# Kernel tuning notes

Hardware: AMD Instinct MI355X
Metric: run time of the kernel (lower is better)

## Reference

```python
import jax, jax.numpy as jnp
import numpy as np

D_MODEL = 1024
NUM_HEADS = 16
NUM_KV_HEADS = 4
HEAD_DIM = D_MODEL // NUM_HEADS  # 64
KV_DIM = HEAD_DIM * NUM_KV_HEADS  # 256
B, N = 2, 2048


def setup_inputs() -> dict:
    key = jax.random.key(0)
    ks = jax.random.split(key, 7)
    std = 1.0 / np.sqrt(D_MODEL)
    return {
        "x": jax.random.normal(ks[0], (B, N, D_MODEL), dtype=jnp.float32),
        "cos": jax.random.uniform(ks[1], (N, HEAD_DIM // 2), dtype=jnp.float32),
        "sin": jax.random.uniform(ks[2], (N, HEAD_DIM // 2), dtype=jnp.float32),
        "Wq": jax.random.normal(ks[3], (D_MODEL, D_MODEL), dtype=jnp.float32) * std,
        "Wk": jax.random.normal(ks[4], (D_MODEL, KV_DIM), dtype=jnp.float32) * std,
        "Wv": jax.random.normal(ks[5], (D_MODEL, KV_DIM), dtype=jnp.float32) * std,
        "Wo": jax.random.normal(ks[6], (D_MODEL, D_MODEL), dtype=jnp.float32) * std,
    }


def _rope(t, cos, sin):
    # t: [B, H, N, head_dim]; cos/sin: [N, head_dim//2]
    t1, t2 = t[..., ::2], t[..., 1::2]
    c = cos[None, None]
    s = sin[None, None]
    # NOTE: halves are concatenated (not re-interleaved), faithful to source.
    return jnp.concatenate([t1 * c - t2 * s, t1 * s + t2 * c], axis=-1)


def reference(x, cos, sin, Wq, Wk, Wv, Wo):
    b, n, d = x.shape
    scale = HEAD_DIM ** -0.5
    q = (x @ Wq).reshape(b, n, NUM_HEADS, HEAD_DIM).transpose(0, 2, 1, 3)
    k = (x @ Wk).reshape(b, n, NUM_KV_HEADS, HEAD_DIM).transpose(0, 2, 1, 3)
    v = (x @ Wv).reshape(b, n, NUM_KV_HEADS, HEAD_DIM).transpose(0, 2, 1, 3)
    q = _rope(q, cos, sin)
    k = _rope(k, cos, sin)
    num_rep = NUM_HEADS // NUM_KV_HEADS
    k = jnp.repeat(k, num_rep, axis=1)  # [b, H, n, hd]
    v = jnp.repeat(v, num_rep, axis=1)
    attn = jnp.einsum("bhqd,bhkd->bhqk", q, k) * scale
    attn = jax.nn.softmax(attn, axis=-1)
    out = jnp.einsum("bhqk,bhkd->bhqd", attn, v)
    out = out.transpose(0, 2, 1, 3).reshape(b, n, d)
    return out @ Wo
```

## Files before the change

kernel.cpp:

```cpp
#include <hip/hip_runtime.h>
#include <math.h>

#define D_MODEL 1024
#define NHEADS  16
#define NKV     4
#define HDIM    64
#define KVDIM   256
#define BB      2
#define NN      2048
#define MROWS   (BB*NN)
#define QKVN    1536
#define NTASK   (MROWS*NHEADS)
#define NSPLIT  2

typedef unsigned short ushort_t;
typedef unsigned int uint_t;
typedef float    f32x4 __attribute__((ext_vector_type(4)));
typedef _Float16 h16x8 __attribute__((ext_vector_type(8)));
typedef _Float16 h16x4 __attribute__((ext_vector_type(4)));
typedef __fp16   fp16x2 __attribute__((ext_vector_type(2)));

#define MFMAH(A,B,C)  __builtin_amdgcn_mfma_f32_16x16x32_f16((A),(B),(C),0,0,0)
#define MFMA16(A,B,C) __builtin_amdgcn_mfma_f32_16x16x16f16((A),(B),(C),0,0,0)
#define EXP2(x) __builtin_amdgcn_exp2f(x)

#define GLDS(gp, lp) __builtin_amdgcn_global_load_lds( \
    (const __attribute__((address_space(1))) void*)(gp), \
    (__attribute__((address_space(3))) void*)(lp), 16, 0, 0)

__device__ __forceinline__ ushort_t f2h(float f) {
    _Float16 h = (_Float16)f;
    return *(ushort_t*)&h;
}
__device__ __forceinline__ float h2f(ushort_t u) {
    return (float)(*(const _Float16*)&u);
}
__device__ __forceinline__ uint_t pk2h(float a, float b) {
    fp16x2 v = __builtin_amdgcn_cvt_pkrtz(a, b);
    return *(uint_t*)&v;
}

__global__ __launch_bounds__(256)
void prep_kernel(const float* __restrict__ x, const float* __restrict__ Wq,
                 const float* __restrict__ Wk, const float* __restrict__ Wv,
                 const float* __restrict__ Wo, ushort_t* __restrict__ xb,
                 ushort_t* __restrict__ WqkvT, ushort_t* __restrict__ WoT)
{
    __shared__ float T[32][33];
    int blk = blockIdx.x;
    if (blk < 4096) {
        const int i = blk * 256 + threadIdx.x;
        float4 v = ((const float4*)x)[i];
        uint2 o;
        o.x = pk2h(v.x, v.y);
        o.y = pk2h(v.z, v.w);
        ((uint2*)xb)[i] = o;
        return;
    }
    blk -= 4096;
    const float* src; ushort_t* dst; int N, bx, by;
    if (blk < 1024)      { src = Wq; dst = WqkvT;                            N = D_MODEL; bx = blk & 31; by = blk >> 5; }
    else if (blk < 1280) { blk -= 1024; src = Wk; dst = WqkvT + (size_t)1024 * D_MODEL; N = KVDIM; bx = blk & 7; by = blk >> 3; }
    else if (blk < 1536) { blk -= 1280; src = Wv; dst = WqkvT + (size_t)1280 * D_MODEL; N = KVDIM; bx = blk & 7; by = blk >> 3; }
    else                 { blk -= 1536; src = Wo; dst = WoT;                 N = D_MODEL; bx = blk & 31; by = blk >> 5; }
    const int tx = threadIdx.x & 31, ty = threadIdx.x >> 5;
    const int n0 = bx * 32, k0 = by * 32;
#pragma unroll
    for (int i = 0; i < 4; i++)
        T[ty + i * 8][tx] = src[(size_t)(k0 + ty + i * 8) * N + n0 + tx];
    __syncthreads();
#pragma unroll
    for (int i = 0; i < 4; i++)
        dst[(size_t)(n0 + ty + i * 8) * D_MODEL + k0 + tx] = f2h(T[tx][ty + i * 8]);
}

__global__ __launch_bounds__(256)
void vtrans_kernel(const ushort_t* __restrict__ QKVh, ushort_t* __restrict__ Vt)
{
    __shared__ ushort_t T[32][34];
    const int tx = threadIdx.x & 31, ty = threadIdx.x >> 5;
    const int n0 = blockIdx.x * 32, d0 = blockIdx.y * 32, b = blockIdx.z;
#pragma unroll
    for (int i = 0; i < 4; i++)
        T[ty + i * 8][tx] =
            QKVh[(size_t)(b * NN + n0 + ty + i * 8) * QKVN + 1280 + d0 + tx];
    __syncthreads();
#pragma unroll
    for (int i = 0; i < 4; i++)
        Vt[(size_t)(b * 256 + d0 + ty + i * 8) * NN + n0 + tx] = T[tx][ty + i * 8];
}

#define NQW (MROWS*NHEADS*32)
#define NKW (MROWS*NKV*32)
__global__ __launch_bounds__(256)
void rope_kernel(const ushort_t* __restrict__ QKVh, const float* __restrict__ Cos,
                 const float* __restrict__ Sin, ushort_t* __restrict__ Qb,
                 ushort_t* __restrict__ Kb)
{
    const float SC = 0.125f * 1.44269504f;
    int idx = blockIdx.x * 256 + threadIdx.x;
    if (idx < NQW) {
        const int row = idx >> 9, rem = idx & 511;
        const int h = rem >> 5, j = rem & 31;
        const int b = row >> 11, n = row & (NN - 1);
        const uint_t pr = *(const uint_t*)&QKVh[(size_t)row * QKVN + h * 64 + 2 * j];
        const float e = h2f((ushort_t)pr), o = h2f((ushort_t)(pr >> 16));
        const float c = Cos[n * 32 + j], s = Sin[n * 32 + j];
        ushort_t* dst = Qb + ((size_t)(b * 16 + h) * NN + n) * 64;
        dst[j]      = f2h((e * c - o * s) * SC);
        dst[j + 32] = f2h((e * s + o * c) * SC);
    } else {
        const int i2 = idx - NQW;
        const int row = i2 >> 7, rem = i2 & 127;
        const int h = rem >> 5, j = rem & 31;
        const int b = row >> 11, n = row & (NN - 1);
        const uint_t pr = *(const uint_t*)&QKVh[(size_t)row * QKVN + 1024 + h * 64 + 2 * j];
        const float e = h2f((ushort_t)pr), o = h2f((ushort_t)(pr >> 16));
        const float c = Cos[n * 32 + j], s = Sin[n * 32 + j];
        ushort_t* dst = Kb + ((size_t)(b * 4 + h) * NN + n) * 64;
        dst[j]      = f2h(e * c - o * s);
        dst[j + 32] = f2h(e * s + o * c);
    }
}

__global__ __launch_bounds__(256)
void gemm_qkv(const ushort_t* __restrict__ A, const ushort_t* __restrict__ Bt,
              ushort_t* __restrict__ C, int M, int N, int K)
{
    __shared__ ushort_t As[2][128 * 32];
    __shared__ ushort_t Bs[2][64 * 32];

    const int tid  = threadIdx.x;
    const int wave = tid >> 6, lane = tid & 63;
    const int quad = lane >> 4, l16 = lane & 15;
    const int rowBase = blockIdx.y * 128, colBase = blockIdx.x * 64;
    const int wm = (wave >> 1) * 64, wn = (wave & 1) * 32;

    f32x4 acc[4][2];
    const f32x4 zz = {0.f, 0.f, 0.f, 0.f};
#pragma unroll
    for (int i = 0; i < 4; i++)
#pragma unroll
        for (int j = 0; j < 2; j++) acc[i][j] = zz;

    const int sr = wave * 32 + (lane >> 2);
    const int sc = ((lane & 3) ^ ((lane >> 3) & 3)) * 8;
    const ushort_t* Ag0 = A + (size_t)(rowBase + sr) * K + sc;
    const ushort_t* Ag1 = A + (size_t)(rowBase + sr + 16) * K + sc;
    const int segA0 = (wave * 2 + 0) * 512, segA1 = (wave * 2 + 1) * 512;
    const int br = wave * 16 + (lane >> 2);
    const ushort_t* Bg0 = Bt + (size_t)(colBase + br) * K + sc;
    const int segB = wave * 512;

    const int fcol = (quad ^ ((l16 >> 1) & 3)) * 8;

    GLDS(Ag0, &As[0][segA0]);
    GLDS(Ag1, &As[0][segA1]);
    GLDS(Bg0, &Bs[0][segB]);

    for (int k0 = 0; k0 < K; k0 += 32) {
        const int cur = (k0 >> 5) & 1, nxt = cur ^ 1;
        __syncthreads();
        if (k0 + 32 < K) {
            GLDS(Ag0 + k0 + 32, &As[nxt][segA0]);
            GLDS(Ag1 + k0 + 32, &As[nxt][segA1]);
            GLDS(Bg0 + k0 + 32, &Bs[nxt][segB]);
        }

        h16x8 af[4], bf[2];
#pragma unroll
        for (int mt = 0; mt < 4; mt++)
            af[mt] = *(const h16x8*)&As[cur][(wm + mt * 16 + l16) * 32 + fcol];
#pragma unroll
        for (int nt = 0; nt < 2; nt++)
            bf[nt] = *(const h16x8*)&Bs[cur][(wn + nt * 16 + l16) * 32 + fcol];
#pragma unroll
        for (int mt = 0; mt < 4; mt++)
#pragma unroll
            for (int nt = 0; nt < 2; nt++)
                acc[mt][nt] = MFMAH(af[mt], bf[nt], acc[mt][nt]);
    }

#pragma unroll
    for (int mt = 0; mt < 4; mt++)
#pragma unroll
        for (int nt = 0; nt < 2; nt++) {
            const int row = rowBase + wm + mt * 16 + quad * 4;
            const int col = colBase + wn + nt * 16 + l16;
#pragma unroll
            for (int r = 0; r < 4; r++)
                C[(size_t)(row + r) * N + col] = f2h(acc[mt][nt][r]);
        }
}

__global__ __launch_bounds__(256)
void attn_mfma(const ushort_t* __restrict__ Qb, const ushort_t* __restrict__ Kb,
               const ushort_t* __restrict__ Vt, ushort_t* __restrict__ Pnum,
               float* __restrict__ Pl)
{
    const int qt = blockIdx.x, h = blockIdx.y;
    const int b = blockIdx.z >> 1, chunk = blockIdx.z & 1;
    const int kvh = h >> 2;
    const int tid = threadIdx.x;
    const int wave = tid >> 6, lane = tid & 63;
    const int quad = lane >> 4, l16 = lane & 15;

    __shared__ ushort_t Ks[64][72];
    __shared__ ushort_t Vs[64][72];

    const int row0 = qt * 256 + wave * 64;
    h16x8 qf[4][2];
#pragma unroll
    for (int mt = 0; mt < 4; mt++) {
        const ushort_t* qp =
            Qb + ((size_t)(b * 16 + h) * NN + row0 + mt * 16 + l16) * 64 + quad * 8;
        qf[mt][0] = *(const h16x8*)qp;
        qf[mt][1] = *(const h16x8*)(qp + 32);
    }

    const ushort_t* kbase = Kb + (size_t)(b * 4 + kvh) * NN * 64;
    const ushort_t* vbase = Vt + (size_t)(b * 256 + kvh * 64) * NN;
    const int key_lo = chunk * (NN / NSPLIT);
    const int rot = (qt + ((h & 3) << 2)) & 15;

    const int srow = tid >> 2, sseg = (tid & 3) * 8;

    const f32x4 zz = {0.f, 0.f, 0.f, 0.f};
    f32x4 o[4][4];
#pragma unroll
    for (int mt = 0; mt < 4; mt++)
#pragma unroll
        for (int dt = 0; dt < 4; dt++) o[mt][dt] = zz;
    float lacc[4] = {0.f, 0.f, 0.f, 0.f};

    int key0 = key_lo + rot * 64;
    const ushort_t* kp0 = kbase + (size_t)(key0 + srow) * 64 + sseg;
    const ushort_t* vp0 = vbase + (size_t)srow * NN + key0 + sseg;
    uint4 kreg0 = *(const uint4*)kp0;
    uint4 kreg1 = *(const uint4*)(kp0 + 32);
    uint4 vreg0 = *(const uint4*)vp0;
    uint4 vreg1 = *(const uint4*)(vp0 + 32);

    for (int t = 0; t < 16; t++) {
        __syncthreads();
        *(uint4*)&Ks[srow][sseg]      = kreg0;
        *(uint4*)&Ks[srow][sseg + 32] = kreg1;
        *(uint4*)&Vs[srow][sseg]      = vreg0;
        *(uint4*)&Vs[srow][sseg + 32] = vreg1;
        __syncthreads();

        if (t < 15) {
            const int kn = key_lo + ((rot + t + 1) & 15) * 64;
            const ushort_t* kpn = kbase + (size_t)(kn + srow) * 64 + sseg;
            const ushort_t* vpn = vbase + (size_t)srow * NN + kn + sseg;
            kreg0 = *(const uint4*)kpn;
            kreg1 = *(const uint4*)(kpn + 32);
            vreg0 = *(const uint4*)vpn;
            vreg1 = *(const uint4*)(vpn + 32);
        }

#pragma unroll
        for (int kt = 0; kt < 4; kt++) {
            h16x8 kf0 = *(const h16x8*)&Ks[kt * 16 + l16][quad * 8];
            h16x8 kf1 = *(const h16x8*)&Ks[kt * 16 + l16][32 + quad * 8];
            h16x4 va[4];
#pragma unroll
            for (int dt = 0; dt < 4; dt++)
                va[dt] = *(const h16x4*)&Vs[dt * 16 + l16][kt * 16 + quad * 4];

            uint2 pb[4];
#pragma unroll
            for (int mt = 0; mt < 4; mt++) {
                f32x4 st = MFMAH(kf0, qf[mt][0], zz);
                st = MFMAH(kf1, qf[mt][1], st);
                const float p0 = EXP2(st[0]);
                const float p1 = EXP2(st[1]);
                const float p2 = EXP2(st[2]);
                const float p3 = EXP2(st[3]);
                lacc[mt] += (p0 + p1) + (p2 + p3);
                pb[mt].x = pk2h(p0, p1);
                pb[mt].y = pk2h(p2, p3);
            }
#pragma unroll
            for (int mt = 0; mt < 4; mt++) {
                const h16x4 pbv = *(const h16x4*)&pb[mt];
#pragma unroll
                for (int dt = 0; dt < 4; dt++)
                    o[mt][dt] = MFMA16(va[dt], pbv, o[mt][dt]);
            }
        }
    }

#pragma unroll
    for (int mt = 0; mt < 4; mt++) {
        lacc[mt] += __shfl_xor(lacc[mt], 16, 64);
        lacc[mt] += __shfl_xor(lacc[mt], 32, 64);
    }

    const size_t task0 = (size_t)(b * 16 + h) * NN + row0;
    ushort_t* np = Pnum + ((size_t)chunk * NTASK + task0) * 64;
#pragma unroll
    for (int mt = 0; mt < 4; mt++) {
        const float inv = 1.0f / lacc[mt];
#pragma unroll
        for (int dt = 0; dt < 4; dt++) {
            f32x4 v = o[mt][dt];
            uint2 pk;
            pk.x = pk2h(v[0] * inv, v[1] * inv);
            pk.y = pk2h(v[2] * inv, v[3] * inv);
            *(uint2*)&np[(size_t)(mt * 16 + l16) * 64 + dt * 16 + quad * 4] = pk;
        }
        if (quad == 0)
            Pl[(size_t)chunk * NTASK + task0 + mt * 16 + l16] = lacc[mt];
    }
}

__global__ __launch_bounds__(256)
void gemm_wo(const ushort_t* __restrict__ Pnum, const float* __restrict__ Pl,
             const ushort_t* __restrict__ WoT, float* __restrict__ C)
{
    __shared__ ushort_t As[2][128 * 40];
    __shared__ ushort_t Bs[2][64 * 32];

    const int tid  = threadIdx.x;
    const int wave = tid >> 6, lane = tid & 63;
    const int quad = lane >> 4, l16 = lane & 15;
    const int rowBase = blockIdx.y * 128, colBase = blockIdx.x * 64;
    const int wm = (wave >> 1) * 64, wn = (wave & 1) * 32;

    f32x4 acc[4][2];
    const f32x4 zz = {0.f, 0.f, 0.f, 0.f};
#pragma unroll
    for (int i = 0; i < 4; i++)
#pragma unroll
        for (int j = 0; j < 2; j++) acc[i][j] = zz;

    const int r0 = tid >> 2;
    const int c8 = (tid & 3) * 8;
    const int bB = rowBase >> 11;
    const int n0 = (rowBase & (NN - 1)) + r0;

    const int br = wave * 16 + (lane >> 2);
    const int sc = ((lane & 3) ^ ((lane >> 3) & 3)) * 8;
    const ushort_t* Bg0 = WoT + (size_t)(colBase + br) * D_MODEL + sc;
    const int segB = wave * 512;
    const int fcol = (quad ^ ((l16 >> 1) & 3)) * 8;

    uint4 a0c0, a0c1, a1c0, a1c1;
    float l00, l01, l10, l11;
#define PREFA(k0) { \
        const int h_ = (k0) >> 6; \
        const int d_ = ((k0) & 63) + c8; \
        const size_t t0_ = ((size_t)(bB * 16 + h_) << 11) + n0; \
        const size_t t1_ = t0_ + 64; \
        a0c0 = *(const uint4*)&Pnum[t0_ * 64 + d_]; \
        a0c1 = *(const uint4*)&Pnum[((size_t)NTASK + t0_) * 64 + d_]; \
        a1c0 = *(const uint4*)&Pnum[t1_ * 64 + d_]; \
        a1c1 = *(const uint4*)&Pnum[((size_t)NTASK + t1_) * 64 + d_]; \
        l00 = Pl[t0_]; l01 = Pl[NTASK + t0_]; \
        l10 = Pl[t1_]; l11 = Pl[NTASK + t1_]; \
    }

    PREFA(0);
    GLDS(Bg0, &Bs[0][segB]);

    for (int k0 = 0; k0 < D_MODEL; k0 += 32) {
        const int cur = (k0 >> 5) & 1, nxt = cur ^ 1;
        __syncthreads();

        {
            const float i0 = 1.f / (l00 + l01), w00 = l00 * i0, w01 = l01 * i0;
            const float i1 = 1.f / (l10 + l11), w10 = l10 * i1, w11 = l11 * i1;
            uint4 o0, o1;
            const uint_t* p0 = (const uint_t*)&a0c0;
            const uint_t* p1 = (const uint_t*)&a0c1;
            const uint_t* q0 = (const uint_t*)&a1c0;
            const uint_t* q1 = (const uint_t*)&a1c1;
            uint_t* po = (uint_t*)&o0;
            uint_t* qo = (uint_t*)&o1;
#pragma unroll
            for (int j = 0; j < 4; j++) {
                fp16x2 u = *(const fp16x2*)&p0[j];
                fp16x2 v = *(const fp16x2*)&p1[j];
                po[j] = pk2h(w00 * (float)u.x + w01 * (float)v.x,
                             w00 * (float)u.y + w01 * (float)v.y);
                fp16x2 s = *(const fp16x2*)&q0[j];
                fp16x2 r = *(const fp16x2*)&q1[j];
                qo[j] = pk2h(w10 * (float)s.x + w11 * (float)r.x,
                             w10 * (float)s.y + w11 * (float)r.y);
            }
            *(uint4*)&As[cur][r0 * 40 + c8]        = o0;
            *(uint4*)&As[cur][(r0 + 64) * 40 + c8] = o1;
        }
        __syncthreads();

        if (k0 + 32 < D_MODEL) {
            GLDS(Bg0 + k0 + 32, &Bs[nxt][segB]);
            PREFA(k0 + 32);
        }

        h16x8 af[4], bf[2];
#pragma unroll
        for (int mt = 0; mt < 4; mt++)
            af[mt] = *(const h16x8*)&As[cur][(wm + mt * 16 + l16) * 40 + quad * 8];
#pragma unroll
        for (int nt = 0; nt < 2; nt++)
            bf[nt] = *(const h16x8*)&Bs[cur][(wn + nt * 16 + l16) * 32 + fcol];
#pragma unroll
        for (int mt = 0; mt < 4; mt++)
#pragma unroll
            for (int nt = 0; nt < 2; nt++)
                acc[mt][nt] = MFMAH(af[mt], bf[nt], acc[mt][nt]);
    }
#undef PREFA

#pragma unroll
    for (int mt = 0; mt < 4; mt++)
#pragma unroll
        for (int nt = 0; nt < 2; nt++) {
            const int row = rowBase + wm + mt * 16 + quad * 4;
            const int col = colBase + wn + nt * 16 + l16;
#pragma unroll
            for (int r = 0; r < 4; r++)
                C[(size_t)(row + r) * D_MODEL + col] = acc[mt][nt][r];
        }
}

extern "C" void kernel_launch(void* const* d_in, const int* in_sizes, int n_in,
                              void* d_out, int out_size, void* d_ws, size_t ws_size,
                              hipStream_t stream)
{
    const float* x    = (const float*)d_in[0];
    const float* cosp = (const float*)d_in[1];
    const float* sinp = (const float*)d_in[2];
    const float* Wq   = (const float*)d_in[3];
    const float* Wk   = (const float*)d_in[4];
    const float* Wv   = (const float*)d_in[5];
    const float* Wo   = (const float*)d_in[6];

    char* w = (char*)d_ws;
    ushort_t* xb     = (ushort_t*)w;                       w += (size_t)MROWS * D_MODEL * 2;
    ushort_t* WqkvT  = (ushort_t*)w;                       w += (size_t)QKVN * D_MODEL * 2;
    ushort_t* WoT    = (ushort_t*)w;                       w += (size_t)D_MODEL * D_MODEL * 2;
    ushort_t* QKVh   = (ushort_t*)w;                       w += (size_t)MROWS * QKVN * 2;
    ushort_t* Qbuf   = (ushort_t*)w;                       w += (size_t)MROWS * D_MODEL * 2;
    ushort_t* Kbuf   = (ushort_t*)w;                       w += (size_t)MROWS * KVDIM * 2;
    ushort_t* Vt     = (ushort_t*)w;                       w += (size_t)MROWS * KVDIM * 2;
    ushort_t* Pnum   = (ushort_t*)w;                       w += (size_t)NSPLIT * NTASK * 64 * 2;
    float*    Pl     = (float*)w;

    prep_kernel<<<6656, 256, 0, stream>>>(x, Wq, Wk, Wv, Wo, xb, WqkvT, WoT);

    gemm_qkv<<<dim3(QKVN / 64, MROWS / 128), 256, 0, stream>>>(
        xb, WqkvT, QKVh, MROWS, QKVN, D_MODEL);

    rope_kernel<<<(NQW + NKW) / 256, 256, 0, stream>>>(QKVh, cosp, sinp, Qbuf, Kbuf);
    vtrans_kernel<<<dim3(NN / 32, KVDIM / 32, BB), 256, 0, stream>>>(QKVh, Vt);

    attn_mfma<<<dim3(NN / 256, NHEADS, BB * NSPLIT), 256, 0, stream>>>(
        Qbuf, Kbuf, Vt, Pnum, Pl);

    gemm_wo<<<dim3(D_MODEL / 64, MROWS / 128), 256, 0, stream>>>(
        Pnum, Pl, WoT, (float*)d_out);
}
```

Measured before the change: 205.6 us.

## Enlarge attention KV tile to 128, MFMA row sums, fuse rope with V transpose

The attention kernel now stages 128 keys per iteration instead of 64, which halves the number of barrier pairs per chunk and doubles the register prefetch depth. The softmax denominator is computed with an extra MFMA against a ones vector instead of scalar adds and cross-lane shuffles. The rope and V-transpose kernels are merged into one launch to save a kernel launch. The trade-off is more LDS per block and more prefetch registers, plus extra MFMA work for the row sums, all of which may reduce occupancy.

After: 194.0 us. 5.7% less time.

```diff
diff --git a/kernel.cpp b/kernel.cpp
--- a/kernel.cpp
+++ b/kernel.cpp
@@ -12,6 +12,8 @@
 #define QKVN    1536
 #define NTASK   (MROWS*NHEADS)
 #define NSPLIT  2
+#define KVBLK   128
+#define NTILE   ((NN/NSPLIT)/KVBLK)
 
 typedef unsigned short ushort_t;
 typedef unsigned int uint_t;
@@ -74,29 +76,30 @@
         dst[(size_t)(n0 + ty + i * 8) * D_MODEL + k0 + tx] = f2h(T[tx][ty + i * 8]);
 }
 
-__global__ __launch_bounds__(256)
-void vtrans_kernel(const ushort_t* __restrict__ QKVh, ushort_t* __restrict__ Vt)
-{
-    __shared__ ushort_t T[32][34];
-    const int tx = threadIdx.x & 31, ty = threadIdx.x >> 5;
-    const int n0 = blockIdx.x * 32, d0 = blockIdx.y * 32, b = blockIdx.z;
-#pragma unroll
-    for (int i = 0; i < 4; i++)
-        T[ty + i * 8][tx] =
-            QKVh[(size_t)(b * NN + n0 + ty + i * 8) * QKVN + 1280 + d0 + tx];
-    __syncthreads();
-#pragma unroll
-    for (int i = 0; i < 4; i++)
-        Vt[(size_t)(b * 256 + d0 + ty + i * 8) * NN + n0 + tx] = T[tx][ty + i * 8];
-}
-
 #define NQW (MROWS*NHEADS*32)
 #define NKW (MROWS*NKV*32)
+#define ROPEBLKS ((NQW + NKW) / 256)
 __global__ __launch_bounds__(256)
-void rope_kernel(const ushort_t* __restrict__ QKVh, const float* __restrict__ Cos,
-                 const float* __restrict__ Sin, ushort_t* __restrict__ Qb,
-                 ushort_t* __restrict__ Kb)
-{
+void ropevt_kernel(const ushort_t* __restrict__ QKVh, const float* __restrict__ Cos,
+                   const float* __restrict__ Sin, ushort_t* __restrict__ Qb,
+                   ushort_t* __restrict__ Kb, ushort_t* __restrict__ Vt)
+{
+    __shared__ ushort_t T[32][34];
+    if (blockIdx.x >= ROPEBLKS) {
+        const int blk2 = blockIdx.x - ROPEBLKS;
+        const int bx = blk2 & 63, by = (blk2 >> 6) & 7, b = blk2 >> 9;
+        const int tx = threadIdx.x & 31, ty = threadIdx.x >> 5;
+        const int n0 = bx * 32, d0 = by * 32;
+#pragma unroll
+        for (int i = 0; i < 4; i++)
+            T[ty + i * 8][tx] =
+                QKVh[(size_t)(b * NN + n0 + ty + i * 8) * QKVN + 1280 + d0 + tx];
+        __syncthreads();
+#pragma unroll
+        for (int i = 0; i < 4; i++)
+            Vt[(size_t)(b * 256 + d0 + ty + i * 8) * NN + n0 + tx] = T[tx][ty + i * 8];
+        return;
+    }
     const float SC = 0.125f * 1.44269504f;
     int idx = blockIdx.x * 256 + threadIdx.x;
     if (idx < NQW) {
@@ -205,8 +208,8 @@
     const int wave = tid >> 6, lane = tid & 63;
     const int quad = lane >> 4, l16 = lane & 15;
 
-    __shared__ ushort_t Ks[64][72];
-    __shared__ ushort_t Vs[64][72];
+    __shared__ ushort_t Ks[128][72];
+    __shared__ ushort_t Vs[64][136];
 
     const int row0 = qt * 256 + wave * 64;
     h16x8 qf[4][2];
@@ -218,12 +221,18 @@
         qf[mt][1] = *(const h16x8*)(qp + 32);
     }
 
+    h16x4 ones;
+#pragma unroll
+    for (int i = 0; i < 4; i++) ones[i] = (_Float16)1.0f;
+
     const ushort_t* kbase = Kb + (size_t)(b * 4 + kvh) * NN * 64;
     const ushort_t* vbase = Vt + (size_t)(b * 256 + kvh * 64) * NN;
     const int key_lo = chunk * (NN / NSPLIT);
-    const int rot = (qt + ((h & 3) << 2)) & 15;
+    const int rot = (qt + ((h & 3) << 2)) & (NTILE - 1);
 
     const int srow = tid >> 2, sseg = (tid & 3) * 8;
+    const ushort_t* kp_lane = kbase + (size_t)srow * 64 + sseg;
+    const ushort_t* vp_lane = vbase + (size_t)srow * NN + sseg;
 
     const f32x4 zz = {0.f, 0.f, 0.f, 0.f};
     f32x4 o[4][4];
@@ -231,36 +240,46 @@
     for (int mt = 0; mt < 4; mt++)
 #pragma unroll
         for (int dt = 0; dt < 4; dt++) o[mt][dt] = zz;
-    float lacc[4] = {0.f, 0.f, 0.f, 0.f};
-
-    int key0 = key_lo + rot * 64;
-    const ushort_t* kp0 = kbase + (size_t)(key0 + srow) * 64 + sseg;
-    const ushort_t* vp0 = vbase + (size_t)srow * NN + key0 + sseg;
-    uint4 kreg0 = *(const uint4*)kp0;
-    uint4 kreg1 = *(const uint4*)(kp0 + 32);
-    uint4 vreg0 = *(const uint4*)vp0;
-    uint4 vreg1 = *(const uint4*)(vp0 + 32);
-
-    for (int t = 0; t < 16; t++) {
-        __syncthreads();
-        *(uint4*)&Ks[srow][sseg]      = kreg0;
-        *(uint4*)&Ks[srow][sseg + 32] = kreg1;
-        *(uint4*)&Vs[srow][sseg]      = vreg0;
-        *(uint4*)&Vs[srow][sseg + 32] = vreg1;
-        __syncthreads();
-
-        if (t < 15) {
-            const int kn = key_lo + ((rot + t + 1) & 15) * 64;
-            const ushort_t* kpn = kbase + (size_t)(kn + srow) * 64 + sseg;
-            const ushort_t* vpn = vbase + (size_t)srow * NN + kn + sseg;
-            kreg0 = *(const uint4*)kpn;
-            kreg1 = *(const uint4*)(kpn + 32);
-            vreg0 = *(const uint4*)vpn;
-            vreg1 = *(const uint4*)(vpn + 32);
-        }
-
-#pragma unroll
-        for (int kt = 0; kt < 4; kt++) {
+    f32x4 lsum[4];
+#pragma unroll
+    for (int mt = 0; mt < 4; mt++) lsum[mt] = zz;
+
+    const int key0 = key_lo + rot * KVBLK;
+    uint4 kreg0 = *(const uint4*)(kp_lane + (size_t)key0 * 64);
+    uint4 kreg1 = *(const uint4*)(kp_lane + (size_t)key0 * 64 + 32);
+    uint4 kreg2 = *(const uint4*)(kp_lane + (size_t)(key0 + 64) * 64);
+    uint4 kreg3 = *(const uint4*)(kp_lane + (size_t)(key0 + 64) * 64 + 32);
+    uint4 vreg0 = *(const uint4*)(vp_lane + key0);
+    uint4 vreg1 = *(const uint4*)(vp_lane + key0 + 32);
+    uint4 vreg2 = *(const uint4*)(vp_lane + key0 + 64);
+    uint4 vreg3 = *(const uint4*)(vp_lane + key0 + 96);
+
+    for (int t = 0; t < NTILE; t++) {
+        __syncthreads();
+        *(uint4*)&Ks[srow][sseg]           = kreg0;
+        *(uint4*)&Ks[srow][sseg + 32]      = kreg1;
+        *(uint4*)&Ks[srow + 64][sseg]      = kreg2;
+        *(uint4*)&Ks[srow + 64][sseg + 32] = kreg3;
+        *(uint4*)&Vs[srow][sseg]           = vreg0;
+        *(uint4*)&Vs[srow][sseg + 32]      = vreg1;
+        *(uint4*)&Vs[srow][sseg + 64]      = vreg2;
+        *(uint4*)&Vs[srow][sseg + 96]      = vreg3;
+        __syncthreads();
+
+        if (t < NTILE - 1) {
+            const int kn = key_lo + ((rot + t + 1) & (NTILE - 1)) * KVBLK;
+            kreg0 = *(const uint4*)(kp_lane + (size_t)kn * 64);
+            kreg1 = *(const uint4*)(kp_lane + (size_t)kn * 64 + 32);
+            kreg2 = *(const uint4*)(kp_lane + (size_t)(kn + 64) * 64);
+            kreg3 = *(const uint4*)(kp_lane + (size_t)(kn + 64) * 64 + 32);
+            vreg0 = *(const uint4*)(vp_lane + kn);
+            vreg1 = *(const uint4*)(vp_lane + kn + 32);
+            vreg2 = *(const uint4*)(vp_lane + kn + 64);
+            vreg3 = *(const uint4*)(vp_lane + kn + 96);
+        }
+
+#pragma unroll
+        for (int kt = 0; kt < 8; kt++) {
             h16x8 kf0 = *(const h16x8*)&Ks[kt * 16 + l16][quad * 8];
             h16x8 kf1 = *(const h16x8*)&Ks[kt * 16 + l16][32 + quad * 8];
             h16x4 va[4];
@@ -273,13 +292,8 @@
             for (int mt = 0; mt < 4; mt++) {
                 f32x4 st = MFMAH(kf0, qf[mt][0], zz);
                 st = MFMAH(kf1, qf[mt][1], st);
-                const float p0 = EXP2(st[0]);
-                const float p1 = EXP2(st[1]);
-                const float p2 = EXP2(st[2]);
-                const float p3 = EXP2(st[3]);
-                lacc[mt] += (p0 + p1) + (p2 + p3);
-                pb[mt].x = pk2h(p0, p1);
-                pb[mt].y = pk2h(p2, p3);
+                pb[mt].x = pk2h(EXP2(st[0]), EXP2(st[1]));
+                pb[mt].y = pk2h(EXP2(st[2]), EXP2(st[3]));
             }
 #pragma unroll
             for (int mt = 0; mt < 4; mt++) {
@@ -287,21 +301,17 @@
 #pragma unroll
                 for (int dt = 0; dt < 4; dt++)
                     o[mt][dt] = MFMA16(va[dt], pbv, o[mt][dt]);
+                lsum[mt] = MFMA16(ones, pbv, lsum[mt]);
             }
         }
-    }
-
-#pragma unroll
-    for (int mt = 0; mt < 4; mt++) {
-        lacc[mt] += __shfl_xor(lacc[mt], 16, 64);
-        lacc[mt] += __shfl_xor(lacc[mt], 32, 64);
     }
 
     const size_t task0 = (size_t)(b * 16 + h) * NN + row0;
     ushort_t* np = Pnum + ((size_t)chunk * NTASK + task0) * 64;
 #pragma unroll
     for (int mt = 0; mt < 4; mt++) {
-        const float inv = 1.0f / lacc[mt];
+        const float lt = lsum[mt][0];
+        const float inv = 1.0f / lt;
 #pragma unroll
         for (int dt = 0; dt < 4; dt++) {
             f32x4 v = o[mt][dt];
@@ -311,7 +321,7 @@
             *(uint2*)&np[(size_t)(mt * 16 + l16) * 64 + dt * 16 + quad * 4] = pk;
         }
         if (quad == 0)
-            Pl[(size_t)chunk * NTASK + task0 + mt * 16 + l16] = lacc[mt];
+            Pl[(size_t)chunk * NTASK + task0 + mt * 16 + l16] = lt;
     }
 }
 
@@ -454,8 +464,8 @@
     gemm_qkv<<<dim3(QKVN / 64, MROWS / 128), 256, 0, stream>>>(
         xb, WqkvT, QKVh, MROWS, QKVN, D_MODEL);
 
-    rope_kernel<<<(NQW + NKW) / 256, 256, 0, stream>>>(QKVh, cosp, sinp, Qbuf, Kbuf);
-    vtrans_kernel<<<dim3(NN / 32, KVDIM / 32, BB), 256, 0, stream>>>(QKVh, Vt);
+    ropevt_kernel<<<ROPEBLKS + 1024, 256, 0, stream>>>(
+        QKVh, cosp, sinp, Qbuf, Kbuf, Vt);
 
     attn_mfma<<<dim3(NN / 256, NHEADS, BB * NSPLIT), 256, 0, stream>>>(
         Qbuf, Kbuf, Vt, Pnum, Pl);
```
